# Performance work log

Hardware: AMD Instinct MI355X
Metric: run time of the kernel (lower is better)

The kernel has to match this reference:

```python
import jax, jax.numpy as jnp
import numpy as np

B, N, C, H = 8, 1025, 1024, 16


def setup_inputs() -> dict:
    key = jax.random.key(0)
    k1, k2, k3, k4 = jax.random.split(key, 4)
    x = jax.random.normal(k1, (B, N, C), dtype=jnp.float32)
    w_qkv = jax.random.normal(k2, (3 * C, C), dtype=jnp.float32) * (C ** -0.5)
    w_proj = jax.random.normal(k3, (C, C), dtype=jnp.float32) * (C ** -0.5)
    b_proj = jax.random.normal(k4, (C,), dtype=jnp.float32) * 0.01
    return {"x": x, "w_qkv": w_qkv, "w_proj": w_proj, "b_proj": b_proj}


def reference(x, w_qkv, w_proj, b_proj):
    b, n, c = x.shape
    hd = c // H
    scale = hd ** -0.5
    qkv = (x @ w_qkv.T).reshape(b, n, 3, H, hd).transpose(2, 0, 3, 1, 4)
    q, k, v = qkv[0], qkv[1], qkv[2]
    # standard QK attention path
    attn_ori = jax.nn.softmax(jnp.einsum('bhnd,bhmd->bhnm', q, k) * scale, axis=-1)
    # CLIP-Surgery V-V self-correlation path (settings='' -> same scale)
    attn_vv = jax.nn.softmax(jnp.einsum('bhnd,bhmd->bhnm', v, v) * scale, axis=-1)
    x_ori = jnp.einsum('bhnm,bhmd->bhnd', attn_ori, v).transpose(0, 2, 1, 3).reshape(b, n, c)
    x_new = jnp.einsum('bhnm,bhmd->bhnd', attn_vv, v).transpose(0, 2, 1, 3).reshape(b, n, c)
    out_vv = x_new @ w_proj.T + b_proj
    out_ori = x_ori @ w_proj.T + b_proj
    return (out_vv, out_ori)
```

## Files before the change

### kernel.cpp

```cpp
#include <hip/hip_runtime.h>

typedef unsigned short ushort_t;
typedef __attribute__((ext_vector_type(8))) __bf16 bf16x8;
typedef __attribute__((ext_vector_type(4))) float f32x4;

constexpr int B_ = 8, N_ = 1025, C_ = 1024, H_ = 16, HD = 64;
constexpr int M_QKV = B_ * N_;
constexpr int M_PROJ = 2 * B_ * N_;
constexpr int K_ = 1024;
constexpr int NT = 1032;
constexpr size_t S1 = (size_t)B_ * H_ * N_ * HD;
constexpr size_t VT_SZ = (size_t)B_ * H_ * HD * NT;

__device__ __forceinline__ ushort_t f2bf(float f) {
    union { float f; unsigned u; } a; a.f = f;
    unsigned r = a.u + 0x7FFFu + ((a.u >> 16) & 1u);
    return (ushort_t)(r >> 16);
}
__device__ __forceinline__ ushort_t f2bf_fast(float f) {
    return (ushort_t)((__float_as_uint(f) + 0x8000u) >> 16);
}
__device__ __forceinline__ unsigned pk2(float x, float y) {
    unsigned a = __float_as_uint(x) + 0x8000u;
    unsigned b = __float_as_uint(y) + 0x8000u;
    return (a >> 16) | (b & 0xffff0000u);
}
__device__ __forceinline__ uint4 pack8(float4 x, float4 y) {
    return make_uint4(pk2(x.x, x.y), pk2(x.z, x.w), pk2(y.x, y.y), pk2(y.z, y.w));
}

union U4 { uint4 v; ushort_t s[8]; };

__device__ __forceinline__ void gload16(const ushort_t* g, ushort_t* l) {
    __builtin_amdgcn_global_load_lds(
        (const __attribute__((address_space(1))) void*)g,
        (__attribute__((address_space(3))) void*)l, 16, 0, 0);
}

__global__ __launch_bounds__(256)
void conv_bf16(const float* __restrict__ src, ushort_t* __restrict__ dst, int n8) {
    const int i = blockIdx.x * 256 + threadIdx.x;
    if (i < n8) {
        const float4* s = (const float4*)src + 2 * (size_t)i;
        ((uint4*)dst)[i] = pack8(s[0], s[1]);
    }
}

__global__ __launch_bounds__(256)
void gemm_qkv(const ushort_t* __restrict__ A, const ushort_t* __restrict__ Bm,
              ushort_t* __restrict__ q, ushort_t* __restrict__ k,
              ushort_t* __restrict__ v, ushort_t* __restrict__ vT) {
    __shared__ ushort_t As[128 * 32];
    __shared__ ushort_t Bs[128 * 32];
    const int tid = threadIdx.x;
    const int wave = tid >> 6, lane = tid & 63;
    const int quad = lane >> 4, l16 = lane & 15;
    const int m0 = blockIdx.y * 128, n0 = blockIdx.x * 128;
    const int wm = (wave & 1) * 64, wn = (wave >> 1) * 64;

    const int col8 = (tid & 3) * 8;
    const int row0 = tid >> 2;
    const int ar0 = min(m0 + row0,      M_QKV - 1);
    const int ar1 = min(m0 + row0 + 64, M_QKV - 1);
    const ushort_t* ga0 = A + (size_t)ar0 * K_ + col8;
    const ushort_t* ga1 = A + (size_t)ar1 * K_ + col8;
    const ushort_t* gb0 = Bm + (size_t)(n0 + row0) * K_ + col8;
    const ushort_t* gb1 = Bm + (size_t)(n0 + row0 + 64) * K_ + col8;
    ushort_t* lA0 = As + tid * 8;
    ushort_t* lA1 = As + (tid + 256) * 8;
    ushort_t* lB0 = Bs + tid * 8;
    ushort_t* lB1 = Bs + (tid + 256) * 8;

    f32x4 acc[4][4] = {};

    for (int k0 = 0; k0 < K_; k0 += 32) {
        __syncthreads();
        gload16(ga0 + k0, lA0);
        gload16(ga1 + k0, lA1);
        gload16(gb0 + k0, lB0);
        gload16(gb1 + k0, lB1);
        __syncthreads();
        bf16x8 af[4], bfr[4];
#pragma unroll
        for (int i = 0; i < 4; i++) {
            af[i]  = *(const bf16x8*)(As + (wm + i * 16 + l16) * 32 + quad * 8);
            bfr[i] = *(const bf16x8*)(Bs + (wn + i * 16 + l16) * 32 + quad * 8);
        }
#pragma unroll
        for (int im = 0; im < 4; im++)
#pragma unroll
            for (int in = 0; in < 4; in++)
                acc[im][in] = __builtin_amdgcn_mfma_f32_16x16x32_bf16(af[im], bfr[in], acc[im][in], 0, 0, 0);
    }

#pragma unroll
    for (int im = 0; im < 4; im++) {
#pragma unroll
        for (int in = 0; in < 4; in++) {
            const int gcol = n0 + wn + in * 16 + l16;
            const int which = gcol >> 10;
            const int c = gcol & 1023;
            const int h = c >> 6, d = c & 63;
            ushort_t* dst = which == 0 ? q : (which == 1 ? k : v);
            const float sc = (which == 0) ? 0.125f : 1.0f;
#pragma unroll
            for (int r = 0; r < 4; r++) {
                const int grow = m0 + wm + im * 16 + quad * 4 + r;
                if (grow < M_QKV) {
                    const int b = grow / N_;
                    const int nn = grow - b * N_;
                    const ushort_t val = f2bf(acc[im][in][r] * sc);
                    const size_t bh = (size_t)(b * H_ + h);
                    dst[(bh * N_ + nn) * HD + d] = val;
                    if (which == 2)
                        vT[(bh * HD + d) * NT + nn] = val;
                }
            }
        }
    }
}

__global__ __launch_bounds__(256, 4)
void attn_kernel(const ushort_t* __restrict__ q, const ushort_t* __restrict__ k,
                 const ushort_t* __restrict__ v, const ushort_t* __restrict__ vT,
                 ushort_t* __restrict__ xvv, ushort_t* __restrict__ xori) {
    __shared__ ushort_t Ks[64][72];
    __shared__ ushort_t Vs[64][72];
    __shared__ ushort_t Vt[64][72];

    const int tid = threadIdx.x;
    const int wave = tid >> 6, lane = tid & 63;
    const int quad = lane >> 4, l16 = lane & 15;
    const int bh = blockIdx.y;
    const int b = bh >> 4, h = bh & 15;

    const size_t base  = (size_t)bh * N_ * HD;
    const size_t baseT = (size_t)bh * HD * NT;
    const int qstart = min((int)blockIdx.x * 64, N_ - 64);
    const int qr0 = qstart + wave * 16;

    ushort_t (*Ps)[72] = Ks;

    bf16x8 qq[2], qv[2];
    {
        const int qrow = qr0 + l16;
#pragma unroll
        for (int kk = 0; kk < 2; kk++) {
            U4 uq, uv;
            uq.v = *(const uint4*)(q + base + (size_t)qrow * HD + kk * 32 + quad * 8);
            uv.v = *(const uint4*)(v + base + (size_t)qrow * HD + kk * 32 + quad * 8);
            qq[kk] = *(const bf16x8*)uq.s;
            qv[kk] = *(const bf16x8*)uv.s;
        }
    }

    float l0a[4] = {0.f, 0.f, 0.f, 0.f}, l1a[4] = {0.f, 0.f, 0.f, 0.f};
    f32x4 o0[4] = {}, o1[4] = {};

    const int srow = tid >> 3;
    const int scc  = (tid & 7) * 8;

    const int nkt = (N_ + 63) / 64;
    for (int kt = 0; kt < nkt; kt++) {
        const int key0 = kt * 64;
        const bool tail = (key0 + 64 > N_);
        __syncthreads();
        if (!tail) {
#pragma unroll
            for (int i = 0; i < 2; i++) {
                const int row = srow + i * 32;
                const int key = key0 + row;
                uint4 kv = *(const uint4*)(k + base + (size_t)key * HD + scc);
                uint4 vv = *(const uint4*)(v + base + (size_t)key * HD + scc);
                uint4 tv = *(const uint4*)(vT + baseT + (size_t)row * NT + key0 + scc);
                *(uint4*)(&Ks[row][scc]) = kv;
                *(uint4*)(&Vs[row][scc]) = vv;
                *(uint4*)(&Vt[row][scc]) = tv;
            }
        } else {
#pragma unroll
            for (int i = 0; i < 2; i++) {
                const int row = srow + i * 32;
                const int key = key0 + row;
                uint4 kv = make_uint4(0, 0, 0, 0), vv = kv;
                if (key < N_) {
                    kv = *(const uint4*)(k + base + (size_t)key * HD + scc);
                    vv = *(const uint4*)(v + base + (size_t)key * HD + scc);
                }
                uint4 tv = *(const uint4*)(vT + baseT + (size_t)row * NT + key0 + scc);
                *(uint4*)(&Ks[row][scc]) = kv;
                *(uint4*)(&Vs[row][scc]) = vv;
                *(uint4*)(&Vt[row][scc]) = tv;
            }
        }
        __syncthreads();

        f32x4 s[4];
#pragma unroll
        for (int t = 0; t < 4; t++) {
            bf16x8 b0 = *(const bf16x8*)(&Ks[t * 16 + l16][quad * 8]);
            bf16x8 b1 = *(const bf16x8*)(&Ks[t * 16 + l16][32 + quad * 8]);
            f32x4 a = {};
            a = __builtin_amdgcn_mfma_f32_16x16x32_bf16(qq[0], b0, a, 0, 0, 0);
            a = __builtin_amdgcn_mfma_f32_16x16x32_bf16(qq[1], b1, a, 0, 0, 0);
            s[t] = a;
        }
        __syncthreads();

        if (tail) {
#pragma unroll
            for (int t = 0; t < 4; t++)
                if (key0 + t * 16 + l16 >= N_) {
#pragma unroll
                    for (int r = 0; r < 4; r++) s[t][r] = -1e30f;
                }
        }
#pragma unroll
        for (int t = 0; t < 4; t++)
#pragma unroll
            for (int r = 0; r < 4; r++) {
                const float p = __expf(s[t][r]);
                l0a[r] += p;
                Ps[wave * 16 + quad * 4 + r][t * 16 + l16] = f2bf_fast(p);
            }
        {
            bf16x8 pa0 = *(const bf16x8*)(&Ps[wave * 16 + l16][quad * 8]);
            bf16x8 pa1 = *(const bf16x8*)(&Ps[wave * 16 + l16][32 + quad * 8]);
#pragma unroll
            for (int t = 0; t < 4; t++) {
                bf16x8 bv0 = *(const bf16x8*)(&Vt[t * 16 + l16][quad * 8]);
                bf16x8 bv1 = *(const bf16x8*)(&Vt[t * 16 + l16][32 + quad * 8]);
                o0[t] = __builtin_amdgcn_mfma_f32_16x16x32_bf16(pa0, bv0, o0[t], 0, 0, 0);
                o0[t] = __builtin_amdgcn_mfma_f32_16x16x32_bf16(pa1, bv1, o0[t], 0, 0, 0);
            }
        }

#pragma unroll
        for (int t = 0; t < 4; t++) {
            bf16x8 b0 = *(const bf16x8*)(&Vs[t * 16 + l16][quad * 8]);
            bf16x8 b1 = *(const bf16x8*)(&Vs[t * 16 + l16][32 + quad * 8]);
            f32x4 a = {};
            a = __builtin_amdgcn_mfma_f32_16x16x32_bf16(qv[0], b0, a, 0, 0, 0);
            a = __builtin_amdgcn_mfma_f32_16x16x32_bf16(qv[1], b1, a, 0, 0, 0);
            s[t] = a;
        }
        if (tail) {
#pragma unroll
            for (int t = 0; t < 4; t++)
                if (key0 + t * 16 + l16 >= N_) {
#pragma unroll
                    for (int r = 0; r < 4; r++) s[t][r] = -1e30f;
                }
        }
#pragma unroll
        for (int t = 0; t < 4; t++)
#pragma unroll
            for (int r = 0; r < 4; r++) {
                const float p = __expf(s[t][r] * 0.125f);
                l1a[r] += p;
                Ps[wave * 16 + quad * 4 + r][t * 16 + l16] = f2bf_fast(p);
            }
        {
            bf16x8 pa0 = *(const bf16x8*)(&Ps[wave * 16 + l16][quad * 8]);
            bf16x8 pa1 = *(const bf16x8*)(&Ps[wave * 16 + l16][32 + quad * 8]);
#pragma unroll
            for (int t = 0; t < 4; t++) {
                bf16x8 bv0 = *(const bf16x8*)(&Vt[t * 16 + l16][quad * 8]);
                bf16x8 bv1 = *(const bf16x8*)(&Vt[t * 16 + l16][32 + quad * 8]);
                o1[t] = __builtin_amdgcn_mfma_f32_16x16x32_bf16(pa0, bv0, o1[t], 0, 0, 0);
                o1[t] = __builtin_amdgcn_mfma_f32_16x16x32_bf16(pa1, bv1, o1[t], 0, 0, 0);
            }
        }
    }

#pragma unroll
    for (int r = 0; r < 4; r++) {
        float L0 = l0a[r], L1 = l1a[r];
#pragma unroll
        for (int off = 1; off < 16; off <<= 1) {
            L0 += __shfl_xor(L0, off);
            L1 += __shfl_xor(L1, off);
        }
        const int row = qr0 + quad * 4 + r;
        const float inv0 = 1.0f / L0;
        const float inv1 = 1.0f / L1;
        const size_t rb = (size_t)(b * N_ + row) * C_ + h * HD;
#pragma unroll
        for (int t = 0; t < 4; t++) {
            const int d = t * 16 + l16;
            xori[rb + d] = f2bf(o0[t][r] * inv0);
            xvv[rb + d]  = f2bf(o1[t][r] * inv1);
        }
    }
}

__global__ __launch_bounds__(256)
void gemm_proj(const ushort_t* __restrict__ A, const ushort_t* __restrict__ Bm,
               const float* __restrict__ bias, float* __restrict__ out) {
    __shared__ ushort_t As[128 * 32];
    __shared__ ushort_t Bs[128 * 32];
    const int tid = threadIdx.x;
    const int wave = tid >> 6, lane = tid & 63;
    const int quad = lane >> 4, l16 = lane & 15;
    const int m0 = blockIdx.y * 128, n0 = blockIdx.x * 128;
    const int wm = (wave & 1) * 64, wn = (wave >> 1) * 64;

    const int col8 = (tid & 3) * 8;
    const int row0 = tid >> 2;
    const int ar0 = min(m0 + row0,      M_PROJ - 1);
    const int ar1 = min(m0 + row0 + 64, M_PROJ - 1);
    const ushort_t* ga0 = A + (size_t)ar0 * K_ + col8;
    const ushort_t* ga1 = A + (size_t)ar1 * K_ + col8;
    const ushort_t* gb0 = Bm + (size_t)(n0 + row0) * K_ + col8;
    const ushort_t* gb1 = Bm + (size_t)(n0 + row0 + 64) * K_ + col8;
    ushort_t* lA0 = As + tid * 8;
    ushort_t* lA1 = As + (tid + 256) * 8;
    ushort_t* lB0 = Bs + tid * 8;
    ushort_t* lB1 = Bs + (tid + 256) * 8;

    f32x4 acc[4][4] = {};

    for (int k0 = 0; k0 < K_; k0 += 32) {
        __syncthreads();
        gload16(ga0 + k0, lA0);
        gload16(ga1 + k0, lA1);
        gload16(gb0 + k0, lB0);
        gload16(gb1 + k0, lB1);
        __syncthreads();
        bf16x8 af[4], bfr[4];
#pragma unroll
        for (int i = 0; i < 4; i++) {
            af[i]  = *(const bf16x8*)(As + (wm + i * 16 + l16) * 32 + quad * 8);
            bfr[i] = *(const bf16x8*)(Bs + (wn + i * 16 + l16) * 32 + quad * 8);
        }
#pragma unroll
        for (int im = 0; im < 4; im++)
#pragma unroll
            for (int in = 0; in < 4; in++)
                acc[im][in] = __builtin_amdgcn_mfma_f32_16x16x32_bf16(af[im], bfr[in], acc[im][in], 0, 0, 0);
    }

#pragma unroll
    for (int im = 0; im < 4; im++) {
#pragma unroll
        for (int in = 0; in < 4; in++) {
            const int gcol = n0 + wn + in * 16 + l16;
            const float bb = bias[gcol];
#pragma unroll
            for (int r = 0; r < 4; r++) {
                const int grow = m0 + wm + im * 16 + quad * 4 + r;
                if (grow < M_PROJ)
                    out[(size_t)grow * C_ + gcol] = acc[im][in][r] + bb;
            }
        }
    }
}

extern "C" void kernel_launch(void* const* d_in, const int* in_sizes, int n_in,
                              void* d_out, int out_size, void* d_ws, size_t ws_size,
                              hipStream_t stream) {
    const float* x      = (const float*)d_in[0];
    const float* w_qkv  = (const float*)d_in[1];
    const float* w_proj = (const float*)d_in[2];
    const float* b_proj = (const float*)d_in[3];
    float* out = (float*)d_out;

    ushort_t* ws = (ushort_t*)d_ws;
    ushort_t* x_bf     = ws;
    ushort_t* xvv      = ws;
    ushort_t* xori     = ws + S1;
    ushort_t* v        = ws + 2 * S1;
    ushort_t* wproj_bf = ws + 2 * S1;

    ushort_t* q        = (ushort_t*)d_out;
    ushort_t* k        = (ushort_t*)d_out + S1;
    ushort_t* vT       = (ushort_t*)d_out + 2 * S1;
    ushort_t* wqkv_bf  = (ushort_t*)d_out + 2 * S1 + VT_SZ;

    {
        const int n8x = (int)(S1 / 8);
        conv_bf16<<<(n8x + 255) / 256, 256, 0, stream>>>(x, x_bf, n8x);
        const int n8w = 3 * C_ * C_ / 8;
        conv_bf16<<<(n8w + 255) / 256, 256, 0, stream>>>(w_qkv, wqkv_bf, n8w);
    }
    {
        dim3 grid(3072 / 128, (M_QKV + 127) / 128);
        gemm_qkv<<<grid, 256, 0, stream>>>(x_bf, wqkv_bf, q, k, v, vT);
    }
    {
        dim3 grid((N_ + 63) / 64, B_ * H_);
        attn_kernel<<<grid, 256, 0, stream>>>(q, k, v, vT, xvv, xori);
    }
    {
        const int n8p = C_ * C_ / 8;
        conv_bf16<<<(n8p + 255) / 256, 256, 0, stream>>>(w_proj, wproj_bf, n8p);
    }
    {
        dim3 grid(1024 / 128, (M_PROJ + 127) / 128);
        gemm_proj<<<grid, 256, 0, stream>>>(xvv, wproj_bf, b_proj, out);
    }
}
```

Measured before the change: 416.4 us.

## Register-prefetch next K/V tiles and give attention its own P buffer

The attention loop now loads the next key tile's K, V and V-transposed data into registers while the current tile is computed, then stores them to shared memory at the top of the next iteration. This hides global load latency behind the MFMA work. A dedicated shared P buffer replaces the aliasing of Ks, which removes the mid-loop barrier. MFMA sections are wrapped in s_setprio to favour matrix issue. The cost is more registers and LDS per block, which may reduce occupancy at launch_bounds(256,4).

```diff
diff --git a/kernel.cpp b/kernel.cpp
--- a/kernel.cpp
+++ b/kernel.cpp
@@ -127,6 +127,7 @@
     __shared__ ushort_t Ks[64][72];
     __shared__ ushort_t Vs[64][72];
     __shared__ ushort_t Vt[64][72];
+    __shared__ ushort_t Ps[64][72];
 
     const int tid = threadIdx.x;
     const int wave = tid >> 6, lane = tid & 63;
@@ -138,8 +139,6 @@
     const size_t baseT = (size_t)bh * HD * NT;
     const int qstart = min((int)blockIdx.x * 64, N_ - 64);
     const int qr0 = qstart + wave * 16;
-
-    ushort_t (*Ps)[72] = Ks;
 
     bf16x8 qq[2], qv[2];
     {
@@ -160,42 +159,44 @@
     const int srow = tid >> 3;
     const int scc  = (tid & 7) * 8;
 
+    uint4 rk[2], rv[2], rt[2];
+#pragma unroll
+    for (int i = 0; i < 2; i++) {
+        const int row = srow + i * 32;
+        rk[i] = *(const uint4*)(k + base + (size_t)row * HD + scc);
+        rv[i] = *(const uint4*)(v + base + (size_t)row * HD + scc);
+        rt[i] = *(const uint4*)(vT + baseT + (size_t)row * NT + scc);
+    }
+
     const int nkt = (N_ + 63) / 64;
     for (int kt = 0; kt < nkt; kt++) {
         const int key0 = kt * 64;
         const bool tail = (key0 + 64 > N_);
-        __syncthreads();
-        if (!tail) {
+
+        __syncthreads();
+#pragma unroll
+        for (int i = 0; i < 2; i++) {
+            const int row = srow + i * 32;
+            *(uint4*)(&Ks[row][scc]) = rk[i];
+            *(uint4*)(&Vs[row][scc]) = rv[i];
+            *(uint4*)(&Vt[row][scc]) = rt[i];
+        }
+        __syncthreads();
+
+        if (kt + 1 < nkt) {
+            const int kn = key0 + 64;
 #pragma unroll
             for (int i = 0; i < 2; i++) {
                 const int row = srow + i * 32;
-                const int key = key0 + row;
-                uint4 kv = *(const uint4*)(k + base + (size_t)key * HD + scc);
-                uint4 vv = *(const uint4*)(v + base + (size_t)key * HD + scc);
-                uint4 tv = *(const uint4*)(vT + baseT + (size_t)row * NT + key0 + scc);
-                *(uint4*)(&Ks[row][scc]) = kv;
-                *(uint4*)(&Vs[row][scc]) = vv;
-                *(uint4*)(&Vt[row][scc]) = tv;
-            }
-        } else {
-#pragma unroll
-            for (int i = 0; i < 2; i++) {
-                const int row = srow + i * 32;
-                const int key = key0 + row;
-                uint4 kv = make_uint4(0, 0, 0, 0), vv = kv;
-                if (key < N_) {
-                    kv = *(const uint4*)(k + base + (size_t)key * HD + scc);
-                    vv = *(const uint4*)(v + base + (size_t)key * HD + scc);
-                }
-                uint4 tv = *(const uint4*)(vT + baseT + (size_t)row * NT + key0 + scc);
-                *(uint4*)(&Ks[row][scc]) = kv;
-                *(uint4*)(&Vs[row][scc]) = vv;
-                *(uint4*)(&Vt[row][scc]) = tv;
-            }
-        }
-        __syncthreads();
+                const int key = min(kn + row, N_ - 1);
+                rk[i] = *(const uint4*)(k + base + (size_t)key * HD + scc);
+                rv[i] = *(const uint4*)(v + base + (size_t)key * HD + scc);
+                rt[i] = *(const uint4*)(vT + baseT + (size_t)row * NT + kn + scc);
+            }
+        }
 
         f32x4 s[4];
+        __builtin_amdgcn_s_setprio(1);
 #pragma unroll
         for (int t = 0; t < 4; t++) {
             bf16x8 b0 = *(const bf16x8*)(&Ks[t * 16 + l16][quad * 8]);
@@ -205,7 +206,7 @@
             a = __builtin_amdgcn_mfma_f32_16x16x32_bf16(qq[1], b1, a, 0, 0, 0);
             s[t] = a;
         }
-        __syncthreads();
+        __builtin_amdgcn_s_setprio(0);
 
         if (tail) {
 #pragma unroll
@@ -226,6 +227,7 @@
         {
             bf16x8 pa0 = *(const bf16x8*)(&Ps[wave * 16 + l16][quad * 8]);
             bf16x8 pa1 = *(const bf16x8*)(&Ps[wave * 16 + l16][32 + quad * 8]);
+            __builtin_amdgcn_s_setprio(1);
 #pragma unroll
             for (int t = 0; t < 4; t++) {
                 bf16x8 bv0 = *(const bf16x8*)(&Vt[t * 16 + l16][quad * 8]);
@@ -233,8 +235,10 @@
                 o0[t] = __builtin_amdgcn_mfma_f32_16x16x32_bf16(pa0, bv0, o0[t], 0, 0, 0);
                 o0[t] = __builtin_amdgcn_mfma_f32_16x16x32_bf16(pa1, bv1, o0[t], 0, 0, 0);
             }
-        }
-
+            __builtin_amdgcn_s_setprio(0);
+        }
+
+        __builtin_amdgcn_s_setprio(1);
 #pragma unroll
         for (int t = 0; t < 4; t++) {
             bf16x8 b0 = *(const bf16x8*)(&Vs[t * 16 + l16][quad * 8]);
@@ -244,6 +248,7 @@
             a = __builtin_amdgcn_mfma_f32_16x16x32_bf16(qv[1], b1, a, 0, 0, 0);
             s[t] = a;
         }
+        __builtin_amdgcn_s_setprio(0);
         if (tail) {
 #pragma unroll
             for (int t = 0; t < 4; t++)
@@ -263,6 +268,7 @@
         {
             bf16x8 pa0 = *(const bf16x8*)(&Ps[wave * 16 + l16][quad * 8]);
             bf16x8 pa1 = *(const bf16x8*)(&Ps[wave * 16 + l16][32 + quad * 8]);
+            __builtin_amdgcn_s_setprio(1);
 #pragma unroll
             for (int t = 0; t < 4; t++) {
                 bf16x8 bv0 = *(const bf16x8*)(&Vt[t * 16 + l16][quad * 8]);
@@ -270,6 +276,7 @@
                 o1[t] = __builtin_amdgcn_mfma_f32_16x16x32_bf16(pa0, bv0, o1[t], 0, 0, 0);
                 o1[t] = __builtin_amdgcn_mfma_f32_16x16x32_bf16(pa1, bv1, o1[t], 0, 0, 0);
             }
+            __builtin_amdgcn_s_setprio(0);
         }
     }
 
```

After: 559.0 us. 34.2% more time.
